# Performance work log

Hardware: AMD Instinct MI355X
Metric: run time of the kernel (lower is better)

Reference implementation:

```python
import jax, jax.numpy as jnp
import numpy as np

N_HEADS = 16
ROPE = 64        # qk_rope_head_dim
KV_LORA = 512
V_DIM = 128
THETA = 10000.0

def rms_norm(x, w, eps=1e-6):
    return x * jax.lax.rsqrt(jnp.mean(x * x, axis=-1, keepdims=True) + eps) * w

def rope_cos_sin(T, d, theta=THETA):
    half = d // 2
    inv = 1.0 / theta ** (jnp.arange(half, dtype=jnp.float32) / half)
    ang = jnp.arange(T, dtype=jnp.float32)[:, None] * inv  # (T, half)
    return jnp.cos(ang), jnp.sin(ang)

def apply_rot(x, cos, sin):
    # x: (B,T,H,D); complex rotation on interleaved pairs
    xr, xi = x[..., 0::2], x[..., 1::2]
    c = cos[None, :, None, :]
    s = sin[None, :, None, :]
    orr = xr * c - xi * s
    oi = xr * s + xi * c
    return jnp.stack([orr, oi], axis=-1).reshape(x.shape)

def setup_inputs() -> dict:
    key = jax.random.key(0)
    ks = jax.random.split(key, 8)
    B, T, C = 2, 2048, 2048
    QLR = 1536
    x = jax.random.normal(ks[0], (B, T, C), dtype=jnp.float32)
    mask = jnp.tril(jnp.ones((T, T), dtype=jnp.int32))[None, None]
    sc = 0.02
    w_qa = jax.random.normal(ks[1], (QLR, C), dtype=jnp.float32) * sc
    qa_norm_w = jnp.ones((QLR,), dtype=jnp.float32)
    w_qb = jax.random.normal(ks[2], (N_HEADS * 2 * ROPE, QLR), dtype=jnp.float32) * sc
    w_kva = jax.random.normal(ks[3], (KV_LORA + ROPE, C), dtype=jnp.float32) * sc
    kva_norm_w = jnp.ones((KV_LORA,), dtype=jnp.float32)
    w_kvb = jax.random.normal(ks[4], (N_HEADS * (ROPE + V_DIM), KV_LORA), dtype=jnp.float32) * sc
    w_o = jax.random.normal(ks[5], (C, N_HEADS * V_DIM), dtype=jnp.float32) * sc
    return {"x": x, "mask": mask, "w_qa": w_qa, "qa_norm_w": qa_norm_w, "w_qb": w_qb,
            "w_kva": w_kva, "kva_norm_w": kva_norm_w, "w_kvb": w_kvb, "w_o": w_o}

def reference(x, mask, w_qa, qa_norm_w, w_qb, w_kva, kva_norm_w, w_kvb, w_o):
    B, T, C = x.shape
    # Q: low-rank compress -> norm -> up-project, split nope/rope halves
    q_c = rms_norm(x @ w_qa.T, qa_norm_w)
    q = (q_c @ w_qb.T).reshape(B, T, N_HEADS, 2 * ROPE)
    q_nope, q_rope = q[..., :ROPE], q[..., ROPE:]
    # KV: joint low-rank + shared rope key
    kv_a = x @ w_kva.T
    kv_c = rms_norm(kv_a[..., :KV_LORA], kva_norm_w)
    k_rope_raw = kv_a[..., KV_LORA:]                       # (B,T,ROPE)
    kv = (kv_c @ w_kvb.T).reshape(B, T, N_HEADS, ROPE + V_DIM)
    k_content, v = kv[..., :ROPE], kv[..., ROPE:]
    k_rope = jnp.broadcast_to(k_rope_raw[:, :, None, :], (B, T, N_HEADS, ROPE))
    cos, sin = rope_cos_sin(T, ROPE)
    q_rope = apply_rot(q_rope, cos, sin)
    k_rope = apply_rot(k_rope, cos, sin)
    q = jnp.concatenate([q_nope, q_rope], axis=-1)         # (B,T,H,2*ROPE)
    k = jnp.concatenate([k_content, k_rope], axis=-1)
    att = jnp.einsum('bqhd,bkhd->bhqk', q, k) * (ROPE ** -0.5)
    att = jnp.where(mask == 0, -jnp.inf, att)
    att = jax.nn.softmax(att, axis=-1)
    # source's nan-guard: uniform attention if any nan appeared
    att = jnp.where(jnp.any(jnp.isnan(att)), jnp.float32(1.0 / T), att)
    out = jnp.einsum('bhqk,bkhd->bqhd', att, v).reshape(B, T, N_HEADS * V_DIM)
    return out @ w_o.T
```

## Files before the change

### kernel.cpp

```cpp
#include <hip/hip_runtime.h>

typedef short bf16x8 __attribute__((ext_vector_type(8)));
typedef unsigned short u16x8 __attribute__((ext_vector_type(8)));
typedef unsigned short u16x4 __attribute__((ext_vector_type(4)));
typedef float f32x4 __attribute__((ext_vector_type(4)));
typedef unsigned u32x4 __attribute__((ext_vector_type(4)));
typedef unsigned u32x2 __attribute__((ext_vector_type(2)));

#define DEV static __device__ __forceinline__

DEV float bf2f(unsigned short u) { return __uint_as_float(((unsigned)u) << 16); }
DEV unsigned short f2bf(float f) {
  unsigned u = __float_as_uint(f);
  return (unsigned short)((u + 0x7fffu + ((u >> 16) & 1u)) >> 16);
}
DEV unsigned cvtpk(float lo, float hi) {
  unsigned r;
  asm("v_cvt_pk_bf16_f32 %0, %1, %2" : "=v"(r) : "v"(lo), "v"(hi));
  return r;
}
DEV void p32swap(unsigned& a, unsigned& b) {
  asm volatile("v_permlane32_swap_b32 %0, %1" : "+v"(a), "+v"(b));
}
DEV void p16swap(unsigned& a, unsigned& b) {
  asm volatile("v_permlane16_swap_b32 %0, %1" : "+v"(a), "+v"(b));
}

#define GLDS16(g, l)                                                                   \
  __builtin_amdgcn_global_load_lds((const __attribute__((address_space(1))) void*)(g), \
                                   (__attribute__((address_space(3))) void*)(l), 16, 0, 0)

DEV void cvt_body(const float* __restrict__ src, unsigned short* __restrict__ dst,
                  int rows, int cols, int dstRows, int bid) {
  int i = bid * 256 + (int)threadIdx.x;
  int e = i << 2;
  int r = e / cols;
  int c = e - r * cols;
  u16x4 o = {0, 0, 0, 0};
  if (r < rows) {
    const float* p = src + (size_t)r * cols + c;
    o[0] = f2bf(p[0]); o[1] = f2bf(p[1]); o[2] = f2bf(p[2]); o[3] = f2bf(p[3]);
  }
  *(u16x4*)(dst + e) = o;
}

__global__ __launch_bounds__(256) void convert_all(
    const float* __restrict__ x, const float* __restrict__ w_qa, const float* __restrict__ w_kva,
    const float* __restrict__ w_qb, const float* __restrict__ w_kvb, const float* __restrict__ w_o,
    unsigned short* __restrict__ xb, unsigned short* __restrict__ wqkva,
    unsigned short* __restrict__ wqbb, unsigned short* __restrict__ wkvbb,
    unsigned short* __restrict__ wob) {
  int bid = blockIdx.x;
  if (bid < 8192)        cvt_body(x,     xb,                        4096, 2048, 4096, bid);
  else if (bid < 11264)  cvt_body(w_qa,  wqkva,                     1536, 2048, 1536, bid - 8192);
  else if (bid < 12544)  cvt_body(w_kva, wqkva + (size_t)1536*2048,  576, 2048,  640, bid - 11264);
  else if (bid < 15616)  cvt_body(w_qb,  wqbb,                      2048, 1536, 2048, bid - 12544);
  else if (bid < 17152)  cvt_body(w_kvb, wkvbb,                     3072,  512, 3072, bid - 15616);
  else                   cvt_body(w_o,   wob,                       2048, 2048, 2048, bid - 17152);
}

template <typename OutT>
DEV void gemm_bt_body(const unsigned short* __restrict__ A, const unsigned short* __restrict__ B,
                      OutT* __restrict__ C, int M, int N, int K, int bidx,
                      unsigned short* As, unsigned short* Bs) {
  const int tid = threadIdx.x;
  const int lane = tid & 63, wave = tid >> 6;
  const int l16 = lane & 15, lhi = lane >> 4;
  const int nbn = N >> 7;
  const int bm = bidx / nbn, bn = bidx - bm * nbn;
  const int m0 = bm << 7, n0 = bn << 7;
  const int wm = (wave >> 1) << 6, wn = (wave & 1) << 6;
  f32x4 acc[4][4] = {};
  for (int k0 = 0; k0 < K; k0 += 64) {
#pragma unroll
    for (int it = 0; it < 4; ++it) {
      int slot = it * 256 + tid;
      int row = slot >> 3, col = (slot & 7) << 3;
      GLDS16(A + (size_t)(m0 + row) * K + k0 + col, As + (it * 256 + wave * 64) * 8);
      GLDS16(B + (size_t)(n0 + row) * K + k0 + col, Bs + (it * 256 + wave * 64) * 8);
    }
    __syncthreads();
#pragma unroll
    for (int ks = 0; ks < 2; ++ks) {
      bf16x8 a[4], b[4];
#pragma unroll
      for (int i = 0; i < 4; ++i) {
        a[i] = *(const bf16x8*)(As + (wm + i * 16 + l16) * 64 + ks * 32 + lhi * 8);
        b[i] = *(const bf16x8*)(Bs + (wn + i * 16 + l16) * 64 + ks * 32 + lhi * 8);
      }
#pragma unroll
      for (int i = 0; i < 4; ++i)
#pragma unroll
        for (int j = 0; j < 4; ++j)
          acc[i][j] = __builtin_amdgcn_mfma_f32_16x16x32_bf16(b[j], a[i], acc[i][j], 0, 0, 0);
    }
    __syncthreads();
  }
#pragma unroll
  for (int i = 0; i < 4; ++i)
#pragma unroll
    for (int j = 0; j < 4; ++j) {
      int row = m0 + wm + i * 16 + l16;
      int col0 = n0 + wn + j * 16 + lhi * 4;
      if constexpr (sizeof(OutT) == 4) {
        f32x4 v = {acc[i][j][0], acc[i][j][1], acc[i][j][2], acc[i][j][3]};
        *(f32x4*)((float*)C + (size_t)row * N + col0) = v;
      } else {
        u32x2 v = {cvtpk(acc[i][j][0], acc[i][j][1]), cvtpk(acc[i][j][2], acc[i][j][3])};
        *(u32x2*)((unsigned short*)C + (size_t)row * N + col0) = v;
      }
    }
}

template <typename OutT>
__global__ __launch_bounds__(256, 2) void gemm_bt(const unsigned short* __restrict__ A,
                                                  const unsigned short* __restrict__ B,
                                                  OutT* __restrict__ C, int M, int N, int K) {
  __shared__ __align__(16) unsigned short As[128 * 64];
  __shared__ __align__(16) unsigned short Bs[128 * 64];
  gemm_bt_body<OutT>(A, B, C, M, N, K, blockIdx.x, As, Bs);
}

DEV void gemm_kvb_body(const unsigned short* __restrict__ A,
                       const unsigned short* __restrict__ B,
                       unsigned short* __restrict__ kvfull,
                       unsigned short* __restrict__ VT,
                       int bidx, unsigned short* As, unsigned short* Bs) {
  const int N = 3072, K = 512;
  const int tid = threadIdx.x;
  const int lane = tid & 63, wave = tid >> 6;
  const int l16 = lane & 15, lhi = lane >> 4;
  const int nbn = N >> 7;
  const int bm = bidx / nbn, bn = bidx - bm * nbn;
  const int m0 = bm << 7, n0 = bn << 7;
  const int wm = (wave >> 1) << 6, wn = (wave & 1) << 6;
  f32x4 acc[4][4] = {};
  for (int k0 = 0; k0 < K; k0 += 64) {
#pragma unroll
    for (int it = 0; it < 4; ++it) {
      int slot = it * 256 + tid;
      int row = slot >> 3, col = (slot & 7) << 3;
      GLDS16(A + (size_t)(m0 + row) * K + k0 + col, As + (it * 256 + wave * 64) * 8);
      GLDS16(B + (size_t)(n0 + row) * K + k0 + col, Bs + (it * 256 + wave * 64) * 8);
    }
    __syncthreads();
#pragma unroll
    for (int ks = 0; ks < 2; ++ks) {
      bf16x8 a[4], b[4];
#pragma unroll
      for (int i = 0; i < 4; ++i) {
        a[i] = *(const bf16x8*)(As + (wm + i * 16 + l16) * 64 + ks * 32 + lhi * 8);
        b[i] = *(const bf16x8*)(Bs + (wn + i * 16 + l16) * 64 + ks * 32 + lhi * 8);
      }
#pragma unroll
      for (int i = 0; i < 4; ++i)
#pragma unroll
        for (int j = 0; j < 4; ++j)
          acc[i][j] = __builtin_amdgcn_mfma_f32_16x16x32_bf16(a[i], b[j], acc[i][j], 0, 0, 0);
    }
    __syncthreads();
  }
#pragma unroll
  for (int i = 0; i < 4; ++i)
#pragma unroll
    for (int j = 0; j < 4; ++j) {
      int col = n0 + wn + j * 16 + l16;
      int h = col / 192;
      int jc = col - h * 192;
      int row0 = m0 + wm + i * 16 + lhi * 4;
      if (jc < 64) {
#pragma unroll
        for (int r = 0; r < 4; ++r)
          kvfull[(size_t)(row0 + r) * 3072 + col] = f2bf(acc[i][j][r]);
      } else {
        int d = jc - 64;
        int b = row0 >> 11, t0 = row0 & 2047;
        u16x4 pk;
#pragma unroll
        for (int r = 0; r < 4; ++r) pk[r] = f2bf(acc[i][j][r]);
        *(u16x4*)(VT + ((size_t)((b * 16 + h) * 128 + d)) * 2048 + t0) = pk;
      }
    }
}

__global__ __launch_bounds__(256, 2) void gemm_up(const unsigned short* __restrict__ q_c,
                                                  const unsigned short* __restrict__ wqbb,
                                                  unsigned short* __restrict__ qfull,
                                                  const unsigned short* __restrict__ kv_c,
                                                  const unsigned short* __restrict__ wkvbb,
                                                  unsigned short* __restrict__ kvfull,
                                                  unsigned short* __restrict__ VT) {
  __shared__ __align__(16) unsigned short As[128 * 64];
  __shared__ __align__(16) unsigned short Bs[128 * 64];
  if (blockIdx.x < 512)
    gemm_bt_body<unsigned short>(q_c, wqbb, qfull, 4096, 2048, 1536, blockIdx.x, As, Bs);
  else
    gemm_kvb_body(kv_c, wkvbb, kvfull, VT, blockIdx.x - 512, As, Bs);
}

__global__ __launch_bounds__(256) void rms_fused(const unsigned short* __restrict__ qkva,
                                                 const float* __restrict__ qw,
                                                 const float* __restrict__ kvw,
                                                 unsigned short* __restrict__ q_c,
                                                 unsigned short* __restrict__ kv_c,
                                                 unsigned short* __restrict__ krope) {
  const int row = blockIdx.x, tid = threadIdx.x;
  const unsigned short* p = qkva + (size_t)row * 2176;
  float fq[8];
  float ssq = 0.f;
  const bool act = tid < 192;
  if (act) {
    u16x8 v = *(const u16x8*)(p + tid * 8);
#pragma unroll
    for (int j = 0; j < 8; ++j) { fq[j] = bf2f(v[j]); ssq += fq[j] * fq[j]; }
  }
  float f0 = bf2f(p[1536 + tid * 2]), f1 = bf2f(p[1536 + tid * 2 + 1]);
  float sskv = f0 * f0 + f1 * f1;
#pragma unroll
  for (int m = 1; m <= 32; m <<= 1) {
    ssq += __shfl_xor(ssq, m);
    sskv += __shfl_xor(sskv, m);
  }
  __shared__ float rq[4], rkv[4];
  if ((tid & 63) == 0) { rq[tid >> 6] = ssq; rkv[tid >> 6] = sskv; }
  __syncthreads();
  float rstdq = rsqrtf((rq[0] + rq[1] + rq[2] + rq[3]) * (1.f / 1536.f) + 1e-6f);
  float rstdkv = rsqrtf((rkv[0] + rkv[1] + rkv[2] + rkv[3]) * (1.f / 512.f) + 1e-6f);
  if (act) {
    u16x8 o;
#pragma unroll
    for (int j = 0; j < 8; ++j) o[j] = f2bf(fq[j] * rstdq * qw[tid * 8 + j]);
    *(u16x8*)(q_c + (size_t)row * 1536 + tid * 8) = o;
  }
  kv_c[(size_t)row * 512 + tid * 2]     = f2bf(f0 * rstdkv * kvw[tid * 2]);
  kv_c[(size_t)row * 512 + tid * 2 + 1] = f2bf(f1 * rstdkv * kvw[tid * 2 + 1]);
  if (tid < 32) {
    int j = tid;
    float xr = bf2f(p[2048 + 2 * j]), xi = bf2f(p[2048 + 2 * j + 1]);
    int t = row & 2047;
    float ang = (float)t * powf(10000.f, -(float)j * (1.f / 32.f));
    float c = cosf(ang), s = sinf(ang);
    krope[(size_t)row * 64 + 2 * j]     = f2bf(xr * c - xi * s);
    krope[(size_t)row * 64 + 2 * j + 1] = f2bf(xr * s + xi * c);
  }
}

__global__ __launch_bounds__(256, 4) void flash_attn(const unsigned short* __restrict__ qfull,
                                                     const unsigned short* __restrict__ kvfull,
                                                     const unsigned short* __restrict__ krope,
                                                     const unsigned short* __restrict__ Vt,
                                                     unsigned short* __restrict__ out) {
  const int tid = threadIdx.x, lane = tid & 63, wave = tid >> 6;
  const int l16 = lane & 15, lhi = lane >> 4;
  const int bid = blockIdx.x;
  const int xcd = bid & 7, Lb = bid >> 3;
  const int bhl = Lb >> 5, cL = Lb & 31;
  const int s = (bhl & 1) ? (31 - cL) : cL;
  const int bh = xcd * 4 + bhl;
  const int h = bh & 15, b = bh >> 4;
  __shared__ __align__(16) unsigned short Ks[64 * 128];
  __shared__ __align__(16) unsigned short Vs[128 * 64];

  const float QSCALE = 0.125f * 1.44269504089f;
  bf16x8 qf[4];
  f32x4 o_acc[8] = {};
  const int qg = s * 64 + wave * 16 + l16;
  {
    const unsigned short* qrow = qfull + (size_t)(b * 2048 + qg) * 2048 + h * 128;
#pragma unroll
    for (int ks = 0; ks < 4; ++ks) {
      u16x8 raw = *(const u16x8*)(qrow + ks * 32 + lhi * 8);
      float f[8];
#pragma unroll
      for (int j = 0; j < 8; ++j) f[j] = bf2f(raw[j]);
      if (ks >= 2) {
#pragma unroll
        for (int pp = 0; pp < 4; ++pp) {
          int d = ks * 32 + lhi * 8 + 2 * pp;
          int jl = (d - 64) >> 1;
          float ang = (float)qg * powf(10000.f, -(float)jl * (1.f / 32.f));
          float co = cosf(ang), si = sinf(ang);
          float xr = f[2 * pp], xi = f[2 * pp + 1];
          f[2 * pp] = xr * co - xi * si;
          f[2 * pp + 1] = xr * si + xi * co;
        }
      }
      bf16x8 fr;
#pragma unroll
      for (int j = 0; j < 8; ++j) fr[j] = (short)f2bf(f[j] * QSCALE);
      qf[ks] = fr;
    }
  }
  float m_run = -1e30f, l_run = 0.f;

  const int bT = b * 2048;
  const unsigned short* Vbh = Vt + (size_t)(b * 16 + h) * 128 * 2048;

  const unsigned short* pK[4];
  const unsigned short* pV[4];
  int sKst[4];
#pragma unroll
  for (int it = 0; it < 4; ++it) {
    int Lo = it * 4096 + wave * 1024 + lane * 16;
    int r = Lo >> 8;
    int w = (Lo & 255) ^ ((r & 7) << 4);
    int cc = w >> 1;
    if (cc < 64) { pK[it] = kvfull + (size_t)(bT + r) * 3072 + h * 192 + cc; sKst[it] = 64 * 3072; }
    else         { pK[it] = krope  + (size_t)(bT + r) * 64 + (cc - 64);      sKst[it] = 64 * 64; }
    int d = Lo >> 7;
    int w2 = (Lo & 127) ^ ((d & 7) << 4);
    pV[it] = Vbh + (size_t)d * 2048 + (w2 >> 1);
  }

  for (int kt = 0; kt <= s; ++kt) {
#pragma unroll
    for (int it = 0; it < 4; ++it) {
      GLDS16(pK[it], Ks + ((it * 4096 + wave * 1024) >> 1));
      pK[it] += sKst[it];
    }
#pragma unroll
    for (int it = 0; it < 4; ++it) {
      GLDS16(pV[it], Vs + ((it * 4096 + wave * 1024) >> 1));
      pV[it] += 64;
    }
    __syncthreads();

    f32x4 st[4] = {};
    __builtin_amdgcn_s_setprio(1);
#pragma unroll
    for (int ks = 0; ks < 4; ++ks) {
#pragma unroll
      for (int nt = 0; nt < 4; ++nt) {
        int row = nt * 16 + l16;
        int byteoff = row * 256 + ((ks * 64 + lhi * 16) ^ ((l16 & 7) << 4));
        bf16x8 kf = *(const bf16x8*)((const char*)Ks + byteoff);
        st[nt] = __builtin_amdgcn_mfma_f32_16x16x32_bf16(kf, qf[ks], st[nt], 0, 0, 0);
      }
    }
    __builtin_amdgcn_s_setprio(0);

    if (kt == s) {
#pragma unroll
      for (int nt = 0; nt < 4; ++nt)
#pragma unroll
        for (int r = 0; r < 4; ++r) {
          int kg = kt * 64 + nt * 16 + lhi * 4 + r;
          st[nt][r] = (kg <= qg) ? st[nt][r] : -1e30f;
        }
    }
    float mx = -1e30f;
#pragma unroll
    for (int nt = 0; nt < 4; ++nt)
#pragma unroll
      for (int r = 0; r < 4; ++r) mx = fmaxf(mx, st[nt][r]);
    mx = fmaxf(mx, __shfl_xor(mx, 16));
    mx = fmaxf(mx, __shfl_xor(mx, 32));
    if (__ballot(mx > m_run + 8.f)) {
      float mnew = fmaxf(m_run, mx);
      float sc = exp2f(m_run - mnew);
      m_run = mnew;
      l_run *= sc;
#pragma unroll
      for (int dt = 0; dt < 8; ++dt) o_acc[dt] *= sc;
    }
    const float mcur = m_run;
    float sum = 0.f;
#pragma unroll
    for (int nt = 0; nt < 4; ++nt)
#pragma unroll
      for (int r = 0; r < 4; ++r) {
        float p = exp2f(st[nt][r] - mcur);
        st[nt][r] = p;
        sum += p;
      }
    sum += __shfl_xor(sum, 16);
    sum += __shfl_xor(sum, 32);
    l_run += sum;
    bf16x8 pw[2];
    {
      unsigned pk01[4], pk23[4];
#pragma unroll
      for (int nt = 0; nt < 4; ++nt) {
        pk01[nt] = cvtpk(st[nt][0], st[nt][1]);
        pk23[nt] = cvtpk(st[nt][2], st[nt][3]);
      }
#pragma unroll
      for (int k2 = 0; k2 < 2; ++k2) {
        unsigned a0 = pk01[2 * k2], b0 = pk01[2 * k2 + 1];
        unsigned a1 = pk23[2 * k2], b1 = pk23[2 * k2 + 1];
        p32swap(a0, b0); p16swap(a0, b0);
        p32swap(a1, b1); p16swap(a1, b1);
        u32x4 t4 = {a0, a1, b0, b1};
        pw[k2] = *(bf16x8*)&t4;
      }
    }

    __builtin_amdgcn_s_setprio(1);
#pragma unroll
    for (int k2 = 0; k2 < 2; ++k2)
#pragma unroll
      for (int dt = 0; dt < 8; ++dt) {
        int row = dt * 16 + l16;
        int byteoff = row * 128 + ((k2 * 64 + lhi * 16) ^ ((l16 & 7) << 4));
        bf16x8 vf = *(const bf16x8*)((const char*)Vs + byteoff);
        o_acc[dt] = __builtin_amdgcn_mfma_f32_16x16x32_bf16(vf, pw[k2], o_acc[dt], 0, 0, 0);
      }
    __builtin_amdgcn_s_setprio(0);

    __syncthreads();
  }

  {
    float inv = 1.0f / l_run;
    unsigned short* orow = out + (size_t)(b * 2048 + qg) * 2048 + h * 128;
#pragma unroll
    for (int dt = 0; dt < 8; ++dt) {
      unsigned w01 = cvtpk(o_acc[dt][0] * inv, o_acc[dt][1] * inv);
      unsigned w23 = cvtpk(o_acc[dt][2] * inv, o_acc[dt][3] * inv);
      u32x2 st2 = {w01, w23};
      *(u32x2*)(orow + dt * 16 + lhi * 4) = st2;
    }
  }
}

extern "C" void kernel_launch(void* const* d_in, const int* in_sizes, int n_in,
                              void* d_out, int out_size, void* d_ws, size_t ws_size,
                              hipStream_t stream) {
  (void)in_sizes; (void)n_in; (void)out_size; (void)ws_size;
  const float* x      = (const float*)d_in[0];
  const float* w_qa   = (const float*)d_in[2];
  const float* qa_nw  = (const float*)d_in[3];
  const float* w_qb   = (const float*)d_in[4];
  const float* w_kva  = (const float*)d_in[5];
  const float* kva_nw = (const float*)d_in[6];
  const float* w_kvb  = (const float*)d_in[7];
  const float* w_o    = (const float*)d_in[8];
  float* out = (float*)d_out;
  char* ws = (char*)d_ws;

  unsigned short* xb     = (unsigned short*)(ws + 0);
  unsigned short* wqkva  = (unsigned short*)(ws + 16777216);
  unsigned short* wqbb   = (unsigned short*)(ws + 25690112);
  unsigned short* wkvbb  = (unsigned short*)(ws + 31981568);
  unsigned short* wob    = (unsigned short*)(ws + 35127296);
  unsigned short* qkva   = (unsigned short*)(ws + 43515904);
  unsigned short* qfull  = (unsigned short*)(ws + 43515904);
  unsigned short* q_c    = (unsigned short*)(ws + 61341696);
  unsigned short* kv_c   = (unsigned short*)(ws + 73924608);
  unsigned short* krope  = (unsigned short*)(ws + 78118912);
  unsigned short* attno  = (unsigned short*)(ws + 61341696);
  unsigned short* Vattn  = (unsigned short*)(ws + 78643200);
  unsigned short* kvfull = (unsigned short*)d_out;

  convert_all<<<21248, 256, 0, stream>>>(x, w_qa, w_kva, w_qb, w_kvb, w_o,
                                         xb, wqkva, wqbb, wkvbb, wob);

  gemm_bt<unsigned short><<<32 * 17, 256, 0, stream>>>(xb, wqkva, qkva, 4096, 2176, 2048);

  rms_fused<<<4096, 256, 0, stream>>>(qkva, qa_nw, kva_nw, q_c, kv_c, krope);

  gemm_up<<<1280, 256, 0, stream>>>(q_c, wqbb, qfull, kv_c, wkvbb, kvfull, Vattn);

  flash_attn<<<1024, 256, 0, stream>>>(qfull, kvfull, krope, Vattn, attno);

  gemm_bt<float><<<32 * 16, 256, 0, stream>>>(attno, wob, out, 4096, 2048, 2048);
}
```

Baseline: 285.3 us.

## Split long causal query tiles across two blocks and merge partials

For query tiles 16-31 the KV range is split in half, and each half runs as its own block. Each block writes unnormalized fp32 partial outputs plus its running max and sum. A new combine kernel merges the two partials with the usual log-sum-exp rescaling. This balances work across blocks, since the longest causal tiles no longer set the tail latency. The cost is 1536 blocks instead of 1024, extra fp32 partial traffic, and one more kernel launch. The partial buffers reuse workspace regions that hold the converted x and weights.

```diff
diff --git a/kernel.cpp b/kernel.cpp
--- a/kernel.cpp
+++ b/kernel.cpp
@@ -249,15 +249,21 @@
                                                      const unsigned short* __restrict__ kvfull,
                                                      const unsigned short* __restrict__ krope,
                                                      const unsigned short* __restrict__ Vt,
-                                                     unsigned short* __restrict__ out) {
+                                                     unsigned short* __restrict__ out,
+                                                     float* __restrict__ O1, float* __restrict__ O2,
+                                                     float* __restrict__ ML1, float* __restrict__ ML2) {
   const int tid = threadIdx.x, lane = tid & 63, wave = tid >> 6;
   const int l16 = lane & 15, lhi = lane >> 4;
   const int bid = blockIdx.x;
   const int xcd = bid & 7, Lb = bid >> 3;
-  const int bhl = Lb >> 5, cL = Lb & 31;
-  const int s = (bhl & 1) ? (31 - cL) : cL;
+  const int bhl = Lb / 48;
+  const int p = Lb - bhl * 48;
   const int bh = xcd * 4 + bhl;
   const int h = bh & 15, b = bh >> 4;
+  int s, kt0, kt1, mode;
+  if (p < 16)      { s = 31 - p; int hs = (s + 1) >> 1; kt0 = hs; kt1 = s + 1; mode = 2; }
+  else if (p < 32) { s = 47 - p; int hs = (s + 1) >> 1; kt0 = 0;  kt1 = hs;    mode = 1; }
+  else             { s = 47 - p; kt0 = 0; kt1 = s + 1; mode = 0; }
   __shared__ __align__(16) unsigned short Ks[64 * 128];
   __shared__ __align__(16) unsigned short Vs[128 * 64];
 
@@ -307,12 +313,13 @@
     int cc = w >> 1;
     if (cc < 64) { pK[it] = kvfull + (size_t)(bT + r) * 3072 + h * 192 + cc; sKst[it] = 64 * 3072; }
     else         { pK[it] = krope  + (size_t)(bT + r) * 64 + (cc - 64);      sKst[it] = 64 * 64; }
+    pK[it] += (size_t)kt0 * sKst[it];
     int d = Lo >> 7;
     int w2 = (Lo & 127) ^ ((d & 7) << 4);
-    pV[it] = Vbh + (size_t)d * 2048 + (w2 >> 1);
-  }
-
-  for (int kt = 0; kt <= s; ++kt) {
+    pV[it] = Vbh + (size_t)d * 2048 + (w2 >> 1) + kt0 * 64;
+  }
+
+  for (int kt = kt0; kt < kt1; ++kt) {
 #pragma unroll
     for (int it = 0; it < 4; ++it) {
       GLDS16(pK[it], Ks + ((it * 4096 + wave * 1024) >> 1));
@@ -369,9 +376,9 @@
     for (int nt = 0; nt < 4; ++nt)
 #pragma unroll
       for (int r = 0; r < 4; ++r) {
-        float p = exp2f(st[nt][r] - mcur);
-        st[nt][r] = p;
-        sum += p;
+        float pv = exp2f(st[nt][r] - mcur);
+        st[nt][r] = pv;
+        sum += pv;
       }
     sum += __shfl_xor(sum, 16);
     sum += __shfl_xor(sum, 32);
@@ -410,7 +417,7 @@
     __syncthreads();
   }
 
-  {
+  if (mode == 0) {
     float inv = 1.0f / l_run;
     unsigned short* orow = out + (size_t)(b * 2048 + qg) * 2048 + h * 128;
 #pragma unroll
@@ -420,7 +427,43 @@
       u32x2 st2 = {w01, w23};
       *(u32x2*)(orow + dt * 16 + lhi * 4) = st2;
     }
-  }
+  } else {
+    float* Op = (mode == 1) ? O1 : O2;
+    float* ML = (mode == 1) ? ML1 : ML2;
+    const int prow = bh * 1024 + (qg - 1024);
+#pragma unroll
+    for (int dt = 0; dt < 8; ++dt)
+      *(f32x4*)(Op + (size_t)prow * 128 + dt * 16 + lhi * 4) = o_acc[dt];
+    if (lhi == 0) { ML[prow * 2] = m_run; ML[prow * 2 + 1] = l_run; }
+  }
+}
+
+__global__ __launch_bounds__(256) void flash_combine(const float* __restrict__ O1,
+                                                     const float* __restrict__ O2,
+                                                     const float* __restrict__ ML1,
+                                                     const float* __restrict__ ML2,
+                                                     unsigned short* __restrict__ out) {
+  int gid = blockIdx.x * 256 + threadIdx.x;
+  int prow = gid >> 4;
+  int d0 = (gid & 15) << 3;
+  float m1 = ML1[prow * 2], l1 = ML1[prow * 2 + 1];
+  float m2 = ML2[prow * 2], l2 = ML2[prow * 2 + 1];
+  float m = fmaxf(m1, m2);
+  float w1 = exp2f(m1 - m), w2 = exp2f(m2 - m);
+  float inv = 1.0f / (l1 * w1 + l2 * w2);
+  const float* a = O1 + (size_t)prow * 128 + d0;
+  const float* c = O2 + (size_t)prow * 128 + d0;
+  f32x4 a0 = *(const f32x4*)a, a1 = *(const f32x4*)(a + 4);
+  f32x4 c0 = *(const f32x4*)c, c1 = *(const f32x4*)(c + 4);
+  u16x8 o;
+#pragma unroll
+  for (int j = 0; j < 4; ++j) {
+    o[j]     = f2bf((a0[j] * w1 + c0[j] * w2) * inv);
+    o[j + 4] = f2bf((a1[j] * w1 + c1[j] * w2) * inv);
+  }
+  int bh = prow >> 10, qr = prow & 1023;
+  int b = bh >> 4, h = bh & 15;
+  *(u16x8*)(out + ((size_t)(b * 2048 + 1024 + qr)) * 2048 + h * 128 + d0) = o;
 }
 
 extern "C" void kernel_launch(void* const* d_in, const int* in_sizes, int n_in,
@@ -451,6 +494,10 @@
   unsigned short* attno  = (unsigned short*)(ws + 61341696);
   unsigned short* Vattn  = (unsigned short*)(ws + 78643200);
   unsigned short* kvfull = (unsigned short*)d_out;
+  float* O1  = (float*)(ws + 0);
+  float* O2  = (float*)(ws + 16777216);
+  float* ML1 = (float*)(ws + 33554432);
+  float* ML2 = (float*)(ws + 33816576);
 
   convert_all<<<21248, 256, 0, stream>>>(x, w_qa, w_kva, w_qb, w_kvb, w_o,
                                          xb, wqkva, wqbb, wkvbb, wob);
@@ -461,7 +508,8 @@
 
   gemm_up<<<1280, 256, 0, stream>>>(q_c, wqbb, qfull, kv_c, wkvbb, kvfull, Vattn);
 
-  flash_attn<<<1024, 256, 0, stream>>>(qfull, kvfull, krope, Vattn, attno);
+  flash_attn<<<1536, 256, 0, stream>>>(qfull, kvfull, krope, Vattn, attno, O1, O2, ML1, ML2);
+  flash_combine<<<2048, 256, 0, stream>>>(O1, O2, ML1, ML2, attno);
 
   gemm_bt<float><<<32 * 16, 256, 0, stream>>>(attno, wob, out, 4096, 2048, 2048);
 }
```

Result: no change. 290.6 us (+1.9%).
